# Kernel optimization log

Hardware: AMD Instinct MI355X
Metric: run time of the kernel (lower is better)

Reference implementation:

```python
import jax, jax.numpy as jnp
import numpy as np

H = 8          # num_heads
NUM_SEEDS = 4  # num_seeds (T = T0 + NUM_SEEDS in training/non_trivial)
NEG_INF = float('-inf')


def setup_inputs() -> dict:
    key = jax.random.key(0)
    ks = jax.random.split(key, 9)
    B, T, L, C = 4, 16, 64, 512
    T0 = T - NUM_SEEDS
    x = jax.random.normal(ks[0], (B, T0 * L, C), dtype=jnp.float32)
    x_ctx = jax.random.normal(ks[1], (B, T, L, C), dtype=jnp.float32)
    dx_ctx = jax.random.normal(ks[2], (B, T, L, C), dtype=jnp.float32)
    ctx_mask = jax.random.randint(ks[3], (B, T), 0, 2).astype(jnp.bool_)
    s = 1.0 / np.sqrt(C)
    qkv_w = jax.random.normal(ks[4], (3 * C, C), dtype=jnp.float32) * s
    k_w = jax.random.normal(ks[5], (C, C), dtype=jnp.float32) * s
    v_w = jax.random.normal(ks[6], (C, C), dtype=jnp.float32) * s
    proj_w = jax.random.normal(ks[7], (C, C), dtype=jnp.float32) * s
    proj_b = jax.random.normal(ks[8], (C,), dtype=jnp.float32) * 0.01
    return {"x": x, "x_ctx": x_ctx, "dx_ctx": dx_ctx, "ctx_mask": ctx_mask,
            "qkv_w": qkv_w, "k_w": k_w, "v_w": v_w, "proj_w": proj_w,
            "proj_b": proj_b}


def reference(x, x_ctx, dx_ctx, ctx_mask, qkv_w, k_w, v_w, proj_w, proj_b):
    B, T, L, C = x_ctx.shape
    T0 = x.shape[1] // L
    hd = C // H
    scale = hd ** (-0.5)

    # qkv for the current (self) tokens: [3, B, H, T0*L, hd]
    qkv = (x @ qkv_w.T).reshape(B, T0 * L, 3, H, hd).transpose(2, 0, 3, 1, 4)
    q, k, v = qkv[0], qkv[1], qkv[2]

    # context keys/values: [B, H, T*L, hd]
    k_ctx = (dx_ctx.reshape(B, T * L, C) @ k_w.T).reshape(B, T * L, H, hd).transpose(0, 2, 1, 3)
    v_ctx = (x_ctx.reshape(B, T * L, C) @ v_w.T).reshape(B, T * L, H, hd).transpose(0, 2, 1, 3)

    # cross-context scores: [B, H, T0*L, T, L]
    attn = (jnp.einsum('bhqd,bhkd->bhqk', q, k_ctx) * scale).reshape(B, H, T0 * L, T, L)

    # context mask: drop whole context frames where ctx_mask is False
    attn = jnp.where(ctx_mask[:, None, None, :, None], attn, NEG_INF)

    # non-trivial temporal mask (training): query frame i can't attend to
    # context frame i + num_seeds
    nt = (jnp.arange(T0)[:, None] + NUM_SEEDS) == jnp.arange(T)[None, :]  # [T0, T]
    attn6 = attn.reshape(B, H, T0, L, T, L)
    attn6 = jnp.where(nt[None, None, :, None, :, None], NEG_INF, attn6)
    attn = attn6.reshape(B, H, T0 * L, T, L)

    # per-frame self attention scores: [B, H, T0, L, L] -> [B, H, T0*L, 1, L]
    q6 = q.reshape(B, H, T0, L, hd)
    k6 = k.reshape(B, H, T0, L, hd)
    self_attn = (jnp.einsum('bhtqd,bhtkd->bhtqk', q6, k6) * scale).reshape(B, H, T0 * L, 1, L)

    # joint softmax over (T+1)*L keys
    attn = jnp.concatenate([attn, self_attn], axis=-2).reshape(B, H, T0 * L, (T + 1) * L)
    attn = jax.nn.softmax(attn, axis=-1)

    # split back: cross part @ v_ctx, self part @ v (per frame)
    out = jnp.einsum('bhqk,bhkd->bhqd', attn[:, :, :, :-L], v_ctx)
    a_self = attn[:, :, :, -L:].reshape(B, H, T0, L, L)
    v6 = v.reshape(B, H, T0, L, hd)
    out = out + jnp.einsum('bhtqk,bhtkd->bhtqd', a_self, v6).reshape(B, H, T0 * L, hd)

    out = out.transpose(0, 2, 1, 3).reshape(B, T0 * L, C)
    return out @ proj_w.T + proj_b
```

## Files before the change

### kernel.cpp

```cpp
#include <hip/hip_runtime.h>
#include <hip/hip_bf16.h>

typedef __attribute__((ext_vector_type(8))) short bf16x8;
typedef __attribute__((ext_vector_type(4))) float f32x4;

#define BB 4
#define TT 16
#define NT0 12
#define LL 64
#define CC 512
#define HH 8
#define HD 64
#define NQ (NT0*LL)
#define NCTX (TT*LL)

#define GPTR(x) ((__attribute__((address_space(1))) void*)(x))
#define SPTR(x) ((__attribute__((address_space(3))) void*)(x))

__device__ __forceinline__ float bf2f(ushort u) {
  union { unsigned int i; float f; } x; x.i = ((unsigned int)u) << 16; return x.f;
}
__device__ __forceinline__ ushort f2bf(float f) {
  union { float f; unsigned int i; } x; x.f = f;
  unsigned int r = x.i + 0x7fffu + ((x.i >> 16) & 1u);
  return (ushort)(r >> 16);
}

__global__ __launch_bounds__(256) void cvt_all(const float* __restrict__ w0,
                                               const float* __restrict__ w1,
                                               const float* __restrict__ w2,
                                               const float* __restrict__ w3,
                                               const float* __restrict__ x,
                                               const float* __restrict__ xc,
                                               const float* __restrict__ dxc,
                                               ushort* __restrict__ dst) {
  long i = (long)blockIdx.x * 256 + threadIdx.x;
  const float* src; long off;
  if (i < 196608)       { src = w0;  off = 0; }
  else if (i < 262144)  { src = w1;  off = 196608; }
  else if (i < 327680)  { src = w2;  off = 262144; }
  else if (i < 393216)  { src = w3;  off = 327680; }
  else if (i < 786432)  { src = x;   off = 393216; }
  else if (i < 1310720) { src = xc;  off = 786432; }
  else                  { src = dxc; off = 1310720; }
  f32x4 v = *(const f32x4*)(src + (i - off) * 4);
  ushort4 o = { f2bf(v[0]), f2bf(v[1]), f2bf(v[2]), f2bf(v[3]) };
  *(ushort4*)(dst + i * 4) = o;
}

__device__ __forceinline__ void gemm128_mac(const ushort* __restrict__ A,
                                            const ushort* __restrict__ W,
                                            int mt, int nt, ushort* lds,
                                            f32x4* acc) {
  int t = threadIdx.x;
  ushort* ldsA = lds;
  ushort* ldsW = lds + 4096;

  int p0 = t, p1 = t + 256;
  int r0 = p0 >> 2, r1 = p1 >> 2;
  int c0 = (p0 & 3) ^ ((r0 >> 1) & 3);
  int c1 = (p1 & 3) ^ ((r1 >> 1) & 3);
  const ushort* ga0 = A + (size_t)(mt * 128 + r0) * 512 + c0 * 8;
  const ushort* ga1 = A + (size_t)(mt * 128 + r1) * 512 + c1 * 8;
  const ushort* gw0 = W + (size_t)(nt * 128 + r0) * 512 + c0 * 8;
  const ushort* gw1 = W + (size_t)(nt * 128 + r1) * 512 + c1 * 8;
  ushort* la0 = ldsA + p0 * 8;
  ushort* la1 = ldsA + p1 * 8;
  ushort* lw0 = ldsW + p0 * 8;
  ushort* lw1 = ldsW + p1 * 8;

  int lane = t & 63, l15 = lane & 15, kg = lane >> 4;
  int wv = t >> 6;
  int mh = (wv >> 1) * 64, nh = (wv & 1) * 64;
  int swz = kg ^ ((l15 >> 1) & 3);
  const ushort* fa = ldsA + (mh + l15) * 32 + swz * 8;
  const ushort* fw = ldsW + (nh + l15) * 32 + swz * 8;

  for (int ks = 0; ks < 16; ++ks) {
    int ko = ks * 32;
    __builtin_amdgcn_global_load_lds(GPTR(ga0 + ko), SPTR(la0), 16, 0, 0);
    __builtin_amdgcn_global_load_lds(GPTR(ga1 + ko), SPTR(la1), 16, 0, 0);
    __builtin_amdgcn_global_load_lds(GPTR(gw0 + ko), SPTR(lw0), 16, 0, 0);
    __builtin_amdgcn_global_load_lds(GPTR(gw1 + ko), SPTR(lw1), 16, 0, 0);
    __syncthreads();
    bf16x8 af[4], wf[4];
#pragma unroll
    for (int i = 0; i < 4; ++i) af[i] = *(const bf16x8*)(fa + i * 512);
#pragma unroll
    for (int i = 0; i < 4; ++i) wf[i] = *(const bf16x8*)(fw + i * 512);
#pragma unroll
    for (int mi = 0; mi < 4; ++mi)
#pragma unroll
      for (int ni = 0; ni < 4; ++ni)
        acc[mi * 4 + ni] =
            __builtin_amdgcn_mfma_f32_16x16x32_bf16(af[mi], wf[ni], acc[mi * 4 + ni], 0, 0, 0);
    __syncthreads();
  }
}

template<int OUTMODE>
__device__ __forceinline__ void gemm128(const ushort* __restrict__ A,
                                        const ushort* __restrict__ W,
                                        ushort* __restrict__ C,
                                        ushort* __restrict__ CT,
                                        float* __restrict__ Cf,
                                        const float* __restrict__ bias,
                                        int mt, int nt, int N, long TM,
                                        ushort* lds) {
  f32x4 acc[16] = {{0,0,0,0},{0,0,0,0},{0,0,0,0},{0,0,0,0},
                   {0,0,0,0},{0,0,0,0},{0,0,0,0},{0,0,0,0},
                   {0,0,0,0},{0,0,0,0},{0,0,0,0},{0,0,0,0},
                   {0,0,0,0},{0,0,0,0},{0,0,0,0},{0,0,0,0}};
  gemm128_mac(A, W, mt, nt, lds, acc);

  int lane = threadIdx.x & 63, l15 = lane & 15, kg = lane >> 4;
  int wv = threadIdx.x >> 6;
  int Rw = mt * 128 + (wv >> 1) * 64;
  int Cw = nt * 128 + (wv & 1) * 64;
#pragma unroll
  for (int mi = 0; mi < 4; ++mi) {
    int row = Rw + mi * 16 + kg * 4;
#pragma unroll
    for (int ni = 0; ni < 4; ++ni) {
      f32x4 v = acc[mi * 4 + ni];
      int col = Cw + ni * 16 + l15;
      if (OUTMODE == 0) {
#pragma unroll
        for (int r = 0; r < 4; ++r) C[(size_t)(row + r) * N + col] = f2bf(v[r]);
      } else if (OUTMODE == 1) {
        ushort4 o = { f2bf(v[0]), f2bf(v[1]), f2bf(v[2]), f2bf(v[3]) };
        *(ushort4*)(CT + (long)col * TM + row) = o;
      } else {
        float bv = bias[col];
#pragma unroll
        for (int r = 0; r < 4; ++r) Cf[(size_t)(row + r) * N + col] = v[r] + bv;
      }
    }
  }
}

__global__ __launch_bounds__(256) void gemm3(const ushort* __restrict__ xb,
                                             const ushort* __restrict__ dxb,
                                             const ushort* __restrict__ xcb,
                                             const ushort* __restrict__ qkvwb,
                                             const ushort* __restrict__ kwb,
                                             const ushort* __restrict__ vwb,
                                             ushort* __restrict__ qkv,
                                             ushort* __restrict__ vselfT,
                                             ushort* __restrict__ kctx,
                                             ushort* __restrict__ vctxT) {
  __shared__ ushort lds[8192];
  int blk = blockIdx.x;
  if (blk < 288) {
    int mt = blk % 24, nt = blk / 24;
    if (nt < 8)
      gemm128<0>(xb, qkvwb, qkv, nullptr, nullptr, nullptr, mt, nt, 1536, 0, lds);
    else
      gemm128<1>(xb, qkvwb, nullptr, vselfT - (size_t)1024 * 3072, nullptr, nullptr,
                 mt, nt, 1536, 3072, lds);
  } else if (blk < 416) {
    int r = blk - 288;
    gemm128<0>(dxb, kwb, kctx, nullptr, nullptr, nullptr, r % 32, r / 32, 512, 0, lds);
  } else {
    int r = blk - 416;
    gemm128<1>(xcb, vwb, nullptr, vctxT, nullptr, nullptr, r % 32, r / 32, 512, 4096, lds);
  }
}

__global__ __launch_bounds__(256) void gemm_proj(const ushort* __restrict__ aout,
                                                 const ushort* __restrict__ pwb,
                                                 const float* __restrict__ bias,
                                                 float* __restrict__ out) {
  __shared__ ushort lds[8192];
  int blk = blockIdx.x;
  gemm128<2>(aout, pwb, nullptr, nullptr, out, bias, blk % 24, blk / 24, 512, 0, lds);
}

__device__ __forceinline__ void attn_tile(const ushort* __restrict__ kbase, int kstr,
                                          const ushort* __restrict__ vtb, int vtN,
                                          bf16x8 q0, bf16x8 q1,
                                          int l15, int kg,
                                          ushort* __restrict__ myPt,
                                          f32x4* acc, float& Lacc) {
  f32x4 s[4];
#pragma unroll
  for (int st = 0; st < 4; ++st) {
    const ushort* kp = kbase + (size_t)(st * 16 + l15) * kstr + kg * 8;
    bf16x8 k0 = *(const bf16x8*)kp;
    bf16x8 k1 = *(const bf16x8*)(kp + 32);
    f32x4 z = {0, 0, 0, 0};
    z = __builtin_amdgcn_mfma_f32_16x16x32_bf16(k0, q0, z, 0, 0, 0);
    z = __builtin_amdgcn_mfma_f32_16x16x32_bf16(k1, q1, z, 0, 0, 0);
    s[st] = z;
  }
#pragma unroll
  for (int st = 0; st < 4; ++st) {
    float p0 = __builtin_exp2f(fmaf(s[st][0], 0.18033688f, -23.0831206f));
    float p1 = __builtin_exp2f(fmaf(s[st][1], 0.18033688f, -23.0831206f));
    float p2 = __builtin_exp2f(fmaf(s[st][2], 0.18033688f, -23.0831206f));
    float p3 = __builtin_exp2f(fmaf(s[st][3], 0.18033688f, -23.0831206f));
    Lacc += (p0 + p1) + (p2 + p3);
    ushort4 pk = { f2bf(p0), f2bf(p1), f2bf(p2), f2bf(p3) };
    *(ushort4*)(myPt + l15 * 72 + st * 16 + kg * 4) = pk;
  }
#pragma unroll
  for (int kc = 0; kc < 2; ++kc) {
    bf16x8 pb = *(const bf16x8*)(myPt + l15 * 72 + kc * 32 + kg * 8);
#pragma unroll
    for (int d = 0; d < 4; ++d) {
      const ushort* vp = vtb + (size_t)(d * 16 + l15) * vtN + kc * 32 + kg * 8;
      bf16x8 vf = *(const bf16x8*)vp;
      acc[d] = __builtin_amdgcn_mfma_f32_16x16x32_bf16(vf, pb, acc[d], 0, 0, 0);
    }
  }
}

__global__ __launch_bounds__(512) void flash_attn(const ushort* __restrict__ qkv,
                                                  const ushort* __restrict__ kctx,
                                                  const ushort* __restrict__ vctxT,
                                                  const ushort* __restrict__ vselfT,
                                                  const int* __restrict__ ctx_mask,
                                                  ushort* __restrict__ aout) {
  __shared__ ushort sm[18432];
  int blk = blockIdx.x;
  int qh = blk & 1;
  int rest = blk >> 1;
  int t0 = rest % NT0;
  int h  = (rest / NT0) % HH;
  int b  = rest / (NT0 * HH);
  int tid = threadIdx.x, wv = tid >> 6, lane = tid & 63;
  int qg = wv & 1, ks = wv >> 1;
  int l15 = lane & 15, kg = lane >> 4;

  int qrow = b * NQ + t0 * LL + qh * 32 + qg * 16 + l15;
  const ushort* qp = qkv + (size_t)qrow * 1536 + h * HD + kg * 8;
  bf16x8 q0 = *(const bf16x8*)qp;
  bf16x8 q1 = *(const bf16x8*)(qp + 32);

  f32x4 acc[4] = {{0,0,0,0},{0,0,0,0},{0,0,0,0},{0,0,0,0}};
  float Lacc = 0.f;
  ushort* Pt0 = sm + wv * 2304;

  int kts[4]; int nkt = 0;
#pragma unroll
  for (int ki = 0; ki < 4; ++ki) {
    int kt = ks * 4 + ki;
    if (ctx_mask[b * TT + kt] != 0 && kt != t0 + 4) kts[nkt++] = kt;
  }

  const ushort* vctxb = vctxT + (size_t)h * HD * (BB * NCTX) + b * NCTX;
  int buf = 0;
  for (int ki = 0; ki < nkt; ++ki) {
    int kt = kts[ki];
    attn_tile(kctx + (size_t)(b * NCTX + kt * LL) * CC + h * HD, CC,
              vctxb + kt * LL, BB * NCTX,
              q0, q1, l15, kg, Pt0 + buf * 1152, acc, Lacc);
    buf ^= 1;
  }
  if (ks == 0) {
    attn_tile(qkv + (size_t)(b * NQ + t0 * LL) * 1536 + CC + h * HD, 1536,
              vselfT + (size_t)h * HD * (BB * NQ) + b * NQ + t0 * LL, BB * NQ,
              q0, q1, l15, kg, Pt0 + buf * 1152, acc, Lacc);
  }

  float Lr = Lacc;
  Lr += __shfl_xor(Lr, 16, 64);
  Lr += __shfl_xor(Lr, 32, 64);

  __syncthreads();
  float* fsm = (float*)sm;
  if (ks) {
    float* reg = fsm + (size_t)(qg * 3 + ks - 1) * 1088;
#pragma unroll
    for (int d = 0; d < 4; ++d) *(f32x4*)(reg + lane * 16 + d * 4) = acc[d];
    reg[1024 + lane] = Lr;
  }
  __syncthreads();
  if (!ks) {
    float Ls = Lr;
    f32x4 o[4];
#pragma unroll
    for (int d = 0; d < 4; ++d) o[d] = acc[d];
#pragma unroll
    for (int j = 0; j < 3; ++j) {
      const float* reg = fsm + (size_t)(qg * 3 + j) * 1088;
      Ls += reg[1024 + lane];
#pragma unroll
      for (int d = 0; d < 4; ++d)
        o[d] += *(const f32x4*)(reg + lane * 16 + d * 4);
    }
    float inv = 1.f / Ls;
    int orow = b * NQ + t0 * LL + qh * 32 + qg * 16 + l15;
#pragma unroll
    for (int d = 0; d < 4; ++d) {
      ushort4 ov = { f2bf(o[d][0] * inv), f2bf(o[d][1] * inv),
                     f2bf(o[d][2] * inv), f2bf(o[d][3] * inv) };
      *(ushort4*)(aout + (size_t)orow * CC + h * HD + d * 16 + kg * 4) = ov;
    }
  }
}

extern "C" void kernel_launch(void* const* d_in, const int* in_sizes, int n_in,
                              void* d_out, int out_size, void* d_ws, size_t ws_size,
                              hipStream_t stream) {
  const float* x        = (const float*)d_in[0];
  const float* x_ctx    = (const float*)d_in[1];
  const float* dx_ctx   = (const float*)d_in[2];
  const int*   ctx_mask = (const int*)d_in[3];
  const float* qkv_w    = (const float*)d_in[4];
  const float* k_w      = (const float*)d_in[5];
  const float* v_w      = (const float*)d_in[6];
  const float* proj_w   = (const float*)d_in[7];
  const float* proj_b   = (const float*)d_in[8];
  float* out = (float*)d_out;

  ushort* ws = (ushort*)d_ws;
  ushort* qkvwb  = ws;
  ushort* kwb    = ws + 786432;
  ushort* vwb    = ws + 1048576;
  ushort* pwb    = ws + 1310720;
  ushort* xb     = ws + 1572864;
  ushort* xcb    = ws + 3145728;
  ushort* dxb    = ws + 5242880;
  ushort* qkv    = ws + 7340032;
  ushort* kctx   = ws + 12058624;
  ushort* vctxT  = ws + 14155776;
  ushort* vselfT = ws + 16252928;
  ushort* aout   = ws + 17825792;

  cvt_all<<<7168, 256, 0, stream>>>(qkv_w, k_w, v_w, proj_w, x, x_ctx, dx_ctx, ws);
  gemm3<<<544, 256, 0, stream>>>(xb, dxb, xcb, qkvwb, kwb, vwb,
                                 qkv, vselfT, kctx, vctxT);
  flash_attn<<<768, 512, 0, stream>>>(qkv, kctx, vctxT, vselfT, ctx_mask, aout);
  gemm_proj<<<96, 256, 0, stream>>>(aout, pwb, proj_b, out);
}
```

Before: 149.8 us.

## Double-buffer LDS tiles in GEMM mainloop to overlap global loads with MFMA

The GEMM inner loop now holds two LDS stages. It issues the direct-to-LDS global loads for the next K slice before computing on the current one, using a vmcnt wait in place of a full drain. This aims to hide global load latency behind the MFMA work in both the projection GEMMs and the QKV GEMMs. In exchange it doubles LDS per block to 32KB, which may reduce occupancy, and it relies on hand-coded waitcnt encoding being correct.

New measurement: 145.7 us. 1.03x faster.

```diff
diff --git a/kernel.cpp b/kernel.cpp
--- a/kernel.cpp
+++ b/kernel.cpp
@@ -16,6 +16,7 @@
 
 #define GPTR(x) ((__attribute__((address_space(1))) void*)(x))
 #define SPTR(x) ((__attribute__((address_space(3))) void*)(x))
+#define VMCNT(n) (((n) & 15) | (((n) >> 4) << 14) | (7u << 4) | (0xFu << 8))
 
 __device__ __forceinline__ float bf2f(ushort u) {
   union { unsigned int i; float f; } x; x.i = ((unsigned int)u) << 16; return x.f;
@@ -53,9 +54,6 @@
                                             int mt, int nt, ushort* lds,
                                             f32x4* acc) {
   int t = threadIdx.x;
-  ushort* ldsA = lds;
-  ushort* ldsW = lds + 4096;
-
   int p0 = t, p1 = t + 256;
   int r0 = p0 >> 2, r1 = p1 >> 2;
   int c0 = (p0 & 3) ^ ((r0 >> 1) & 3);
@@ -64,25 +62,39 @@
   const ushort* ga1 = A + (size_t)(mt * 128 + r1) * 512 + c1 * 8;
   const ushort* gw0 = W + (size_t)(nt * 128 + r0) * 512 + c0 * 8;
   const ushort* gw1 = W + (size_t)(nt * 128 + r1) * 512 + c1 * 8;
-  ushort* la0 = ldsA + p0 * 8;
-  ushort* la1 = ldsA + p1 * 8;
-  ushort* lw0 = ldsW + p0 * 8;
-  ushort* lw1 = ldsW + p1 * 8;
 
   int lane = t & 63, l15 = lane & 15, kg = lane >> 4;
   int wv = t >> 6;
   int mh = (wv >> 1) * 64, nh = (wv & 1) * 64;
   int swz = kg ^ ((l15 >> 1) & 3);
-  const ushort* fa = ldsA + (mh + l15) * 32 + swz * 8;
-  const ushort* fw = ldsW + (nh + l15) * 32 + swz * 8;
-
+  int faoff = (mh + l15) * 32 + swz * 8;
+  int fwoff = (nh + l15) * 32 + swz * 8;
+
+  __builtin_amdgcn_global_load_lds(GPTR(ga0), SPTR(lds + p0 * 8), 16, 0, 0);
+  __builtin_amdgcn_global_load_lds(GPTR(ga1), SPTR(lds + p1 * 8), 16, 0, 0);
+  __builtin_amdgcn_global_load_lds(GPTR(gw0), SPTR(lds + 4096 + p0 * 8), 16, 0, 0);
+  __builtin_amdgcn_global_load_lds(GPTR(gw1), SPTR(lds + 4096 + p1 * 8), 16, 0, 0);
+
+#pragma unroll
   for (int ks = 0; ks < 16; ++ks) {
-    int ko = ks * 32;
-    __builtin_amdgcn_global_load_lds(GPTR(ga0 + ko), SPTR(la0), 16, 0, 0);
-    __builtin_amdgcn_global_load_lds(GPTR(ga1 + ko), SPTR(la1), 16, 0, 0);
-    __builtin_amdgcn_global_load_lds(GPTR(gw0 + ko), SPTR(lw0), 16, 0, 0);
-    __builtin_amdgcn_global_load_lds(GPTR(gw1 + ko), SPTR(lw1), 16, 0, 0);
-    __syncthreads();
+    int cur = (ks & 1) * 8192;
+    int nxt = 8192 - cur;
+    if (ks < 15) {
+      int ko = (ks + 1) * 32;
+      __builtin_amdgcn_global_load_lds(GPTR(ga0 + ko), SPTR(lds + nxt + p0 * 8), 16, 0, 0);
+      __builtin_amdgcn_global_load_lds(GPTR(ga1 + ko), SPTR(lds + nxt + p1 * 8), 16, 0, 0);
+      __builtin_amdgcn_global_load_lds(GPTR(gw0 + ko), SPTR(lds + nxt + 4096 + p0 * 8), 16, 0, 0);
+      __builtin_amdgcn_global_load_lds(GPTR(gw1 + ko), SPTR(lds + nxt + 4096 + p1 * 8), 16, 0, 0);
+      __builtin_amdgcn_s_waitcnt(VMCNT(4));
+    } else {
+      __builtin_amdgcn_s_waitcnt(VMCNT(0));
+    }
+    asm volatile("" ::: "memory");
+    __builtin_amdgcn_s_barrier();
+    asm volatile("" ::: "memory");
+
+    const ushort* fa = lds + cur + faoff;
+    const ushort* fw = lds + cur + 4096 + fwoff;
     bf16x8 af[4], wf[4];
 #pragma unroll
     for (int i = 0; i < 4; ++i) af[i] = *(const bf16x8*)(fa + i * 512);
@@ -94,7 +106,10 @@
       for (int ni = 0; ni < 4; ++ni)
         acc[mi * 4 + ni] =
             __builtin_amdgcn_mfma_f32_16x16x32_bf16(af[mi], wf[ni], acc[mi * 4 + ni], 0, 0, 0);
-    __syncthreads();
+
+    asm volatile("" ::: "memory");
+    __builtin_amdgcn_s_barrier();
+    asm volatile("" ::: "memory");
   }
 }
 
@@ -149,7 +164,7 @@
                                              ushort* __restrict__ vselfT,
                                              ushort* __restrict__ kctx,
                                              ushort* __restrict__ vctxT) {
-  __shared__ ushort lds[8192];
+  __shared__ ushort lds[16384];
   int blk = blockIdx.x;
   if (blk < 288) {
     int mt = blk % 24, nt = blk / 24;
@@ -171,7 +186,7 @@
                                                  const ushort* __restrict__ pwb,
                                                  const float* __restrict__ bias,
                                                  float* __restrict__ out) {
-  __shared__ ushort lds[8192];
+  __shared__ ushort lds[16384];
   int blk = blockIdx.x;
   gemm128<2>(aout, pwb, nullptr, nullptr, out, bias, blk % 24, blk / 24, 512, 0, lds);
 }
```
